# Optimization experiments

Measured on AMD Instinct MI355X. Metric: run time of the kernel, lower is better.

The kernel has to match this reference:

```python
import jax, jax.numpy as jnp
import numpy as np

EPS = 1e-8  # torch.nn.CosineSimilarity default eps


def setup_inputs() -> dict:
    key = jax.random.key(0)
    k1, k2 = jax.random.split(key)
    input1 = jax.random.normal(k1, (8192, 128), dtype=jnp.float32)
    input2 = jax.random.normal(k2, (8192, 128), dtype=jnp.float32)
    return {"input1": input1, "input2": input2}


def reference(input1, input2):
    # Pairwise cosine similarity [N, M]:
    # sim = <x, y> / max(||x|| * ||y||, eps)  (matches torch CosineSimilarity)
    dots = jnp.einsum("nd,md->nm", input1, input2)          # [N, M]
    n1 = jnp.linalg.norm(input1, axis=-1)                    # [N]
    n2 = jnp.linalg.norm(input2, axis=-1)                    # [M]
    denom = jnp.maximum(n1[:, None] * n2[None, :], EPS)      # [N, M]
    return dots / denom
```

## Files before the change

kernel.cpp:

```cpp
#include <hip/hip_runtime.h>
#include <hip/hip_bf16.h>

#define NROWS 8192
#define DDIM 128

typedef __attribute__((ext_vector_type(8))) short bf16x8;
typedef __attribute__((ext_vector_type(4))) float f32x4;

__global__ __launch_bounds__(256) void prep_kernel(
    const float* __restrict__ in1, const float* __restrict__ in2,
    __hip_bfloat16* __restrict__ Apk, __hip_bfloat16* __restrict__ Bpk,
    float* __restrict__ rn1, float* __restrict__ rn2) {
  int gw = (blockIdx.x * 256 + threadIdx.x) >> 6;
  int l = threadIdx.x & 63;
  int row;
  const float* src;
  char* dstbase;
  float* nrm;
  if (gw < NROWS) {
    row = gw;
    src = in1 + (size_t)row * DDIM;
    dstbase = (char*)Apk;
    nrm = rn1 + row;
  } else {
    row = gw - NROWS;
    src = in2 + (size_t)row * DDIM;
    dstbase = (char*)Bpk;
    nrm = rn2 + row;
  }
  float2 v = ((const float2*)src)[l];
  float s = v.x * v.x + v.y * v.y;
  __hip_bfloat162 h;
  h.x = __float2bfloat16(v.x);
  h.y = __float2bfloat16(v.y);

  int rb = row >> 4, ri = row & 15;
  int sk = l >> 4;
  int q2 = (l & 15) >> 2;
  int j2 = l & 3;
  char* dst = dstbase + (size_t)(rb * 4 + sk) * 1024 + ri * 64 + q2 * 16 + j2 * 4;
  *(__hip_bfloat162*)dst = h;

#pragma unroll
  for (int off = 1; off < 64; off <<= 1) s += __shfl_xor(s, off);
  if (l == 0) *nrm = 1.0f / sqrtf(s);
}

__global__ __launch_bounds__(256, 3) void cos_gemm(
    const __hip_bfloat16* __restrict__ Apk, const __hip_bfloat16* __restrict__ Bpk,
    const float* __restrict__ rn1, const float* __restrict__ rn2,
    float* __restrict__ out) {
  const int tid = threadIdx.x;
  const int l = tid & 63;
  const int w = tid >> 6;
  const int q = l >> 4;
  const int c16 = l & 15;
  const int wr = w >> 1, wc = w & 1;
  const int brow = blockIdx.x * 128;
  const int bcol = blockIdx.y * 128;

  const char* Ap = (const char*)Apk;
  const char* Bp = (const char*)Bpk;
  const int rb0a = (brow >> 4) + wr * 4;
  const int rb0b = (bcol >> 4) + wc * 4;
  const int laneoff = c16 * 64 + q * 16;

  f32x4 acc[4][4] = {};

#pragma unroll
  for (int s = 0; s < 4; ++s) {
    bf16x8 af[4], bfr[4];
#pragma unroll
    for (int m = 0; m < 4; ++m) {
      af[m]  = *(const bf16x8*)(Ap + (size_t)((rb0a + m) * 4 + s) * 1024 + laneoff);
      bfr[m] = *(const bf16x8*)(Bp + (size_t)((rb0b + m) * 4 + s) * 1024 + laneoff);
    }
#pragma unroll
    for (int m = 0; m < 4; ++m)
#pragma unroll
      for (int n = 0; n < 4; ++n)
        acc[m][n] =
            __builtin_amdgcn_mfma_f32_16x16x32_bf16(bfr[n], af[m], acc[m][n], 0, 0, 0);
  }

  float r1v[4];
#pragma unroll
  for (int m = 0; m < 4; ++m) r1v[m] = rn1[brow + wr * 64 + m * 16 + c16];
  float4 r2v[4];
#pragma unroll
  for (int n = 0; n < 4; ++n)
    r2v[n] = *(const float4*)&rn2[bcol + wc * 64 + n * 16 + q * 4];

#pragma unroll
  for (int m = 0; m < 4; ++m) {
    size_t rowoff = (size_t)(brow + wr * 64 + m * 16 + c16) * NROWS;
#pragma unroll
    for (int n = 0; n < 4; ++n) {
      float4 v;
      v.x = acc[m][n][0] * r1v[m] * r2v[n].x;
      v.y = acc[m][n][1] * r1v[m] * r2v[n].y;
      v.z = acc[m][n][2] * r1v[m] * r2v[n].z;
      v.w = acc[m][n][3] * r1v[m] * r2v[n].w;
      *(float4*)&out[rowoff + bcol + wc * 64 + n * 16 + q * 4] = v;
    }
  }
}

extern "C" void kernel_launch(void* const* d_in, const int* in_sizes, int n_in,
                              void* d_out, int out_size, void* d_ws, size_t ws_size,
                              hipStream_t stream) {
  const float* in1 = (const float*)d_in[0];
  const float* in2 = (const float*)d_in[1];
  float* out = (float*)d_out;
  char* ws = (char*)d_ws;

  __hip_bfloat16* Apk = (__hip_bfloat16*)(ws);
  __hip_bfloat16* Bpk = (__hip_bfloat16*)(ws + (size_t)NROWS * DDIM * 2);
  float* rn1 = (float*)(ws + (size_t)NROWS * DDIM * 4);
  float* rn2 = (float*)(ws + (size_t)NROWS * DDIM * 4 + NROWS * 4);

  prep_kernel<<<dim3(16384 / 4), 256, 0, stream>>>(in1, in2, Apk, Bpk, rn1, rn2);
  cos_gemm<<<dim3(64, 64), 256, 0, stream>>>(Apk, Bpk, rn1, rn2, out);
}
```

Baseline: 75.74 us.

## Stage GEMM tiles in LDS, remap blocks per XCD, coalesce output via LDS

The GEMM now copies the A and B tiles into LDS with async global-to-LDS loads, where before each wave read them straight from global memory. Blocks are remapped on a 1D grid so each XCD handles a band of rows, which improves L2 reuse of A. The output tile is transposed through swizzled LDS so each row is written as full contiguous 512-byte segments with nontemporal stores. The 64KB of LDS per block limits occupancy, and launch bounds drop from 3 to 2 blocks, in exchange for better coalescing on the 256MB output write.

```diff
diff --git a/kernel.cpp b/kernel.cpp
--- a/kernel.cpp
+++ b/kernel.cpp
@@ -46,34 +46,52 @@
   if (l == 0) *nrm = 1.0f / sqrtf(s);
 }
 
-__global__ __launch_bounds__(256, 3) void cos_gemm(
+__device__ inline void async_load16(const void* g, void* l) {
+  __builtin_amdgcn_global_load_lds(
+      (const __attribute__((address_space(1))) void*)g,
+      (__attribute__((address_space(3))) void*)l, 16, 0, 0);
+}
+
+__global__ __launch_bounds__(256, 2) void cos_gemm(
     const __hip_bfloat16* __restrict__ Apk, const __hip_bfloat16* __restrict__ Bpk,
     const float* __restrict__ rn1, const float* __restrict__ rn2,
     float* __restrict__ out) {
+  __shared__ char lds[64 * 1024];
+  char* lA = lds;
+  char* lB = lds + 32 * 1024;
+
   const int tid = threadIdx.x;
   const int l = tid & 63;
   const int w = tid >> 6;
   const int q = l >> 4;
   const int c16 = l & 15;
   const int wr = w >> 1, wc = w & 1;
-  const int brow = blockIdx.x * 128;
-  const int bcol = blockIdx.y * 128;
 
-  const char* Ap = (const char*)Apk;
-  const char* Bp = (const char*)Bpk;
-  const int rb0a = (brow >> 4) + wr * 4;
-  const int rb0b = (bcol >> 4) + wc * 4;
+  int wg = blockIdx.x;
+  int xcd = wg & 7;
+  int c = wg >> 3;
+  const int brow = (xcd * 8 + (c >> 6)) * 128;
+  const int bcol = (c & 63) * 128;
+
+  const char* Ag = (const char*)Apk + (size_t)(brow >> 4) * 4096;
+  const char* Bg = (const char*)Bpk + (size_t)(bcol >> 4) * 4096;
+#pragma unroll
+  for (int i = 0; i < 8; ++i) {
+    int f = w * 8 + i;
+    async_load16(Ag + f * 1024 + l * 16, lA + f * 1024);
+    async_load16(Bg + f * 1024 + l * 16, lB + f * 1024);
+  }
+  __syncthreads();
+
   const int laneoff = c16 * 64 + q * 16;
-
   f32x4 acc[4][4] = {};
-
 #pragma unroll
   for (int s = 0; s < 4; ++s) {
     bf16x8 af[4], bfr[4];
 #pragma unroll
     for (int m = 0; m < 4; ++m) {
-      af[m]  = *(const bf16x8*)(Ap + (size_t)((rb0a + m) * 4 + s) * 1024 + laneoff);
-      bfr[m] = *(const bf16x8*)(Bp + (size_t)((rb0b + m) * 4 + s) * 1024 + laneoff);
+      af[m]  = *(const bf16x8*)(lA + ((wr * 4 + m) * 4 + s) * 1024 + laneoff);
+      bfr[m] = *(const bf16x8*)(lB + ((wc * 4 + m) * 4 + s) * 1024 + laneoff);
     }
 #pragma unroll
     for (int m = 0; m < 4; ++m)
@@ -82,6 +100,8 @@
         acc[m][n] =
             __builtin_amdgcn_mfma_f32_16x16x32_bf16(bfr[n], af[m], acc[m][n], 0, 0, 0);
   }
+
+  __syncthreads();
 
   float r1v[4];
 #pragma unroll
@@ -93,16 +113,27 @@
 
 #pragma unroll
   for (int m = 0; m < 4; ++m) {
-    size_t rowoff = (size_t)(brow + wr * 64 + m * 16 + c16) * NROWS;
+    int row = wr * 64 + m * 16 + c16;
 #pragma unroll
     for (int n = 0; n < 4; ++n) {
-      float4 v;
-      v.x = acc[m][n][0] * r1v[m] * r2v[n].x;
-      v.y = acc[m][n][1] * r1v[m] * r2v[n].y;
-      v.z = acc[m][n][2] * r1v[m] * r2v[n].z;
-      v.w = acc[m][n][3] * r1v[m] * r2v[n].w;
-      *(float4*)&out[rowoff + bcol + wc * 64 + n * 16 + q * 4] = v;
+      int g = wc * 16 + n * 4 + q;
+      f32x4 v;
+      v[0] = acc[m][n][0] * r1v[m] * r2v[n].x;
+      v[1] = acc[m][n][1] * r1v[m] * r2v[n].y;
+      v[2] = acc[m][n][2] * r1v[m] * r2v[n].z;
+      v[3] = acc[m][n][3] * r1v[m] * r2v[n].w;
+      *(f32x4*)(lds + (size_t)row * 512 + ((g ^ (row & 31)) * 16)) = v;
     }
+  }
+  __syncthreads();
+
+#pragma unroll
+  for (int i = 0; i < 16; ++i) {
+    int row = w * 32 + i * 2 + (l >> 5);
+    int g = l & 31;
+    f32x4 v = *(const f32x4*)(lds + (size_t)row * 512 + ((g ^ (row & 31)) * 16));
+    __builtin_nontemporal_store(
+        v, (f32x4*)(out + (size_t)(brow + row) * NROWS + bcol + g * 4));
   }
 }
 
@@ -120,5 +151,5 @@
   float* rn2 = (float*)(ws + (size_t)NROWS * DDIM * 4 + NROWS * 4);
 
   prep_kernel<<<dim3(16384 / 4), 256, 0, stream>>>(in1, in2, Apk, Bpk, rn1, rn2);
-  cos_gemm<<<dim3(64, 64), 256, 0, stream>>>(Apk, Bpk, rn1, rn2, out);
+  cos_gemm<<<dim3(4096), 256, 0, stream>>>(Apk, Bpk, rn1, rn2, out);
 }
```

Result: faster. 65.98 us (-12.9%).
